# Kernel tuning notes

Hardware: AMD Instinct MI355X
Metric: run time of the kernel (lower is better)

## Reference

```python
import jax, jax.numpy as jnp
import numpy as np

B = 256          # graphs per batch
N = 128          # nodes per graph (equal-size graphs; batch is block-contiguous)
P = N * (N - 1) // 2  # pairs per graph = 8128
E = B * 1024     # total edges
D = 128          # node feature dim
L = 32           # latent dim

# precomputed local upper-triangular pair indices (constants)
_PI, _PJ = np.triu_indices(N, k=1)
_PI = jnp.asarray(_PI); _PJ = jnp.asarray(_PJ)


def setup_inputs() -> dict:
    key = jax.random.key(0)
    ks = jax.random.split(key, 8)
    x = jax.random.normal(ks[0], (B * N, D), dtype=jnp.float32)
    # within-graph edges with local i < j
    li = jax.random.randint(ks[1], (E,), 0, N - 1)
    r = jax.random.randint(ks[2], (E,), 0, 1 << 30)
    lj = li + 1 + r % (N - 1 - li)
    g = jax.random.randint(ks[3], (E,), 0, B)
    off = g * N
    edge_index = jnp.stack([off + li, off + lj]).astype(jnp.int64)
    batch = jnp.repeat(jnp.arange(B), N).astype(jnp.int64)
    eps = jax.random.normal(ks[4], (B * N, L), dtype=jnp.float32)
    W1 = jax.random.normal(ks[5], (D, D), dtype=jnp.float32) * 0.05
    b1 = jnp.zeros((D,), dtype=jnp.float32)
    Wmu = jax.random.normal(ks[6], (D, L), dtype=jnp.float32) * 0.05
    bmu = jnp.zeros((L,), dtype=jnp.float32)
    Wls = jax.random.normal(ks[7], (D, L), dtype=jnp.float32) * 0.05
    bls = jnp.zeros((L,), dtype=jnp.float32)
    return {"x": x, "edge_index": edge_index, "batch": batch, "eps": eps,
            "W1": W1, "b1": b1, "Wmu": Wmu, "bmu": bmu, "Wls": Wls, "bls": bls}


def reference(x, edge_index, batch, eps, W1, b1, Wmu, bmu, Wls, bls):
    src, dst = edge_index[0], edge_index[1]
    # --- encoder: one symmetric message-passing layer -> Gaussian q per node ---
    agg = jnp.zeros_like(x).at[dst].add(x[src]).at[src].add(x[dst])
    h = jax.nn.relu((x + agg) @ W1 + b1)
    mu = h @ Wmu + bmu                       # [BN, L]
    log_std = h @ Wls + bls
    std = jnp.exp(log_std)
    z = mu + std * eps                       # rsample
    # --- KL(q || N(0,I)) per node, summed per graph (kls[b]) ---
    kl_node = 0.5 * jnp.sum(std * std + mu * mu - 1.0 - 2.0 * log_std, axis=-1)
    kls = jax.ops.segment_sum(kl_node, batch, num_segments=B)  # [B]
    # --- link targets: scatter edges into triangular pair slots ---
    li, lj, be = src % N, dst % N, src // N
    pidx = li * (2 * N - li - 1) // 2 + (lj - li - 1)
    targets = jnp.zeros((B, P), dtype=z.dtype).at[be, pidx].set(1.0)
    # --- inner-product Bernoulli decoder over all pairs of every graph ---
    zb = z.reshape(B, N, L)
    logits = jnp.einsum('bpl,bpl->bp', zb[:, _PI], zb[:, _PJ])   # [B, P]
    log_probs = jnp.sum(targets * logits - jax.nn.softplus(logits), axis=-1)  # [B]
    elbo = jnp.mean(log_probs - kls)
    return -elbo
```

## Files before the change

kernel.cpp:

```cpp
#include <hip/hip_runtime.h>
#include <math.h>

#define B_ 256
#define N_ 128
#define D_ 128
#define L_ 32
#define E_ 262144
#define PW_ 254
#define DCAP 96

#define NDEG_OFF 0
#define BM_OFF   32768
#define KLS_OFF  97792
#define LP_OFF   98048
#define ADJ_OFF  98304
#define Z_OFF    884736
#define ZERO_WORDS 98304

__global__ __launch_bounds__(256) void k_build(
    const int* __restrict__ ei, unsigned* __restrict__ ndeg,
    unsigned char* __restrict__ adj, unsigned* __restrict__ bm)
{
    int e = blockIdx.x * 256 + threadIdx.x;
    int src = ei[e], dst = ei[E_ + e];
    unsigned s1 = atomicAdd(&ndeg[src], 1u);
    if (s1 < DCAP) adj[(size_t)src * DCAP + s1] = (unsigned char)(dst & 127);
    unsigned s2 = atomicAdd(&ndeg[dst], 1u);
    if (s2 < DCAP) adj[(size_t)dst * DCAP + s2] = (unsigned char)(src & 127);
    int li = src & 127, lj = dst & 127, g = src >> 7;
    int p = li * (255 - li) / 2 + (lj - li - 1);
    atomicOr(&bm[g * PW_ + (p >> 5)], 1u << (p & 31));
}

__global__ __launch_bounds__(256, 4) void k_encoder(
    const float* __restrict__ x, const unsigned* __restrict__ ndeg,
    const unsigned char* __restrict__ adj,
    const float* __restrict__ W1, const float* __restrict__ b1,
    const float* __restrict__ Wmu, const float* __restrict__ bmu,
    const float* __restrict__ Wls, const float* __restrict__ bls,
    const float* __restrict__ eps,
    float* __restrict__ z, float* __restrict__ kls)
{
    __shared__ float XAs[32 * 132];
    __shared__ float Ws[4096];
    int t = threadIdx.x;
    int g = blockIdx.x & 255;
    int quar = blockIdx.x >> 8;
    int row0 = g * 128 + quar * 32;
    int rg = t >> 5;
    int cg = t & 31;
    int lane = t & 63;

    {
        int nidx = t >> 4;
        int fo = (t & 15) * 8;
        for (int p = 0; p < 2; ++p) {
            int lrow = p * 16 + nidx;
            int gnode = row0 + lrow;
            const float* xr = x + (size_t)gnode * 128 + fo;
            float4 a0 = *(const float4*)xr;
            float4 a1 = *(const float4*)(xr + 4);
            int deg = (int)ndeg[gnode];
            if (deg > DCAP) deg = DCAP;
            const unsigned char* al = adj + (size_t)gnode * DCAP;
            const float* gx = x + (size_t)(gnode & ~127) * 128 + fo;
            int e = 0;
            for (; e + 4 <= deg; e += 4) {
                unsigned pk = *(const unsigned*)(al + e);
                const float* r0 = gx + (pk & 255u) * 128;
                const float* r1 = gx + ((pk >> 8) & 255u) * 128;
                const float* r2 = gx + ((pk >> 16) & 255u) * 128;
                const float* r3 = gx + (pk >> 24) * 128;
                float4 v00 = *(const float4*)r0, v01 = *(const float4*)(r0 + 4);
                float4 v10 = *(const float4*)r1, v11 = *(const float4*)(r1 + 4);
                float4 v20 = *(const float4*)r2, v21 = *(const float4*)(r2 + 4);
                float4 v30 = *(const float4*)r3, v31 = *(const float4*)(r3 + 4);
                a0.x += v00.x + v10.x + v20.x + v30.x;
                a0.y += v00.y + v10.y + v20.y + v30.y;
                a0.z += v00.z + v10.z + v20.z + v30.z;
                a0.w += v00.w + v10.w + v20.w + v30.w;
                a1.x += v01.x + v11.x + v21.x + v31.x;
                a1.y += v01.y + v11.y + v21.y + v31.y;
                a1.z += v01.z + v11.z + v21.z + v31.z;
                a1.w += v01.w + v11.w + v21.w + v31.w;
            }
            for (; e < deg; ++e) {
                const float* r = gx + (unsigned)al[e] * 128;
                float4 v0 = *(const float4*)r, v1 = *(const float4*)(r + 4);
                a0.x += v0.x; a0.y += v0.y; a0.z += v0.z; a0.w += v0.w;
                a1.x += v1.x; a1.y += v1.y; a1.z += v1.z; a1.w += v1.w;
            }
            *(float4*)(XAs + lrow * 132 + fo) = a0;
            *(float4*)(XAs + lrow * 132 + fo + 4) = a1;
        }
    }
    __syncthreads();

    float acc[4][4];
    #pragma unroll
    for (int i = 0; i < 4; ++i)
        #pragma unroll
        for (int j = 0; j < 4; ++j) acc[i][j] = 0.f;

    for (int kq = 0; kq < 4; ++kq) {
        if (kq) __syncthreads();
        #pragma unroll
        for (int i = 0; i < 4; ++i) {
            int c = t + i * 256;
            ((float4*)Ws)[c] = ((const float4*)(W1 + kq * 4096))[c];
        }
        __syncthreads();
        #pragma unroll 2
        for (int k = 0; k < 32; k += 4) {
            float4 av[4], wv[4];
            #pragma unroll
            for (int i = 0; i < 4; ++i)
                av[i] = *(const float4*)(XAs + (4 * rg + i) * 132 + kq * 32 + k);
            #pragma unroll
            for (int dk = 0; dk < 4; ++dk)
                wv[dk] = *(const float4*)(Ws + (k + dk) * 128 + 4 * cg);
            #pragma unroll
            for (int i = 0; i < 4; ++i) {
                acc[i][0] += av[i].x * wv[0].x + av[i].y * wv[1].x + av[i].z * wv[2].x + av[i].w * wv[3].x;
                acc[i][1] += av[i].x * wv[0].y + av[i].y * wv[1].y + av[i].z * wv[2].y + av[i].w * wv[3].y;
                acc[i][2] += av[i].x * wv[0].z + av[i].y * wv[1].z + av[i].z * wv[2].z + av[i].w * wv[3].z;
                acc[i][3] += av[i].x * wv[0].w + av[i].y * wv[1].w + av[i].z * wv[2].w + av[i].w * wv[3].w;
            }
        }
    }
    __syncthreads();

    {
        float4 bb = *(const float4*)(b1 + 4 * cg);
        #pragma unroll
        for (int i = 0; i < 4; ++i) {
            float4 h;
            h.x = fmaxf(acc[i][0] + bb.x, 0.f);
            h.y = fmaxf(acc[i][1] + bb.y, 0.f);
            h.z = fmaxf(acc[i][2] + bb.z, 0.f);
            h.w = fmaxf(acc[i][3] + bb.w, 0.f);
            *(float4*)(XAs + (4 * rg + i) * 132 + 4 * cg) = h;
        }
    }

    float a3[4][2];
    #pragma unroll
    for (int i = 0; i < 4; ++i) { a3[i][0] = 0.f; a3[i][1] = 0.f; }

    for (int kh = 0; kh < 2; ++kh) {
        __syncthreads();
        #pragma unroll
        for (int i = 0; i < 4; ++i) {
            int c = t + i * 256;
            int row = c >> 4, col4 = (c & 15) << 2;
            int rowg = kh * 64 + row;
            float4 v = (col4 < 32) ? *(const float4*)(Wmu + rowg * 32 + col4)
                                   : *(const float4*)(Wls + rowg * 32 + col4 - 32);
            *(float4*)(Ws + row * 64 + col4) = v;
        }
        __syncthreads();
        #pragma unroll 2
        for (int k = 0; k < 64; k += 4) {
            float4 av[4];
            float2 wv[4];
            #pragma unroll
            for (int i = 0; i < 4; ++i)
                av[i] = *(const float4*)(XAs + (4 * rg + i) * 132 + kh * 64 + k);
            #pragma unroll
            for (int dk = 0; dk < 4; ++dk)
                wv[dk] = *(const float2*)(Ws + (k + dk) * 64 + 2 * cg);
            #pragma unroll
            for (int i = 0; i < 4; ++i) {
                a3[i][0] += av[i].x * wv[0].x + av[i].y * wv[1].x + av[i].z * wv[2].x + av[i].w * wv[3].x;
                a3[i][1] += av[i].x * wv[0].y + av[i].y * wv[1].y + av[i].z * wv[2].y + av[i].w * wv[3].y;
            }
        }
    }
    {
        float2 bv = (cg < 16) ? *(const float2*)(bmu + 2 * cg)
                              : *(const float2*)(bls + 2 * cg - 32);
        #pragma unroll
        for (int i = 0; i < 4; ++i) { a3[i][0] += bv.x; a3[i][1] += bv.y; }
    }

    float o3[4][2];
    #pragma unroll
    for (int i = 0; i < 4; ++i) {
        o3[i][0] = __shfl_xor(a3[i][0], 16);
        o3[i][1] = __shfl_xor(a3[i][1], 16);
    }

    float klsum = 0.f;
    if (cg < 16) {
        int lo = cg;
        #pragma unroll
        for (int i = 0; i < 4; ++i) {
            int rowg = row0 + 4 * rg + i;
            float mu0 = a3[i][0], mu1 = a3[i][1];
            float ls0 = o3[i][0], ls1 = o3[i][1];
            float2 ev = *(const float2*)(eps + (size_t)rowg * 32 + 2 * lo);
            float s0 = __expf(ls0), s1 = __expf(ls1);
            float2 zv = make_float2(mu0 + s0 * ev.x, mu1 + s1 * ev.y);
            *(float2*)(z + (size_t)rowg * 32 + 2 * lo) = zv;
            klsum += s0 * s0 + mu0 * mu0 - 1.f - 2.f * ls0
                   + s1 * s1 + mu1 * mu1 - 1.f - 2.f * ls1;
        }
    }
    #pragma unroll
    for (int off = 32; off > 0; off >>= 1) klsum += __shfl_xor(klsum, off);
    if (lane == 0) atomicAdd(&kls[g], 0.5f * klsum);
}

__global__ __launch_bounds__(256) void k_decoder(
    const float* __restrict__ z, const unsigned* __restrict__ bitmap,
    float* __restrict__ logp)
{
    __shared__ float zT[32 * 132];
    __shared__ unsigned bm[PW_];
    int b = blockIdx.x & 255, quar = blockIdx.x >> 8, t = threadIdx.x;

    #pragma unroll
    for (int i = 0; i < 16; ++i) {
        int c = t + i * 256;
        int n = c >> 5, l = c & 31;
        zT[l * 132 + n] = z[((size_t)b * N_ + n) * L_ + l];
    }
    if (t < PW_) bm[t] = bitmap[b * PW_ + t];
    __syncthreads();

    int i0 = quar * 32 + ((t >> 5) << 2);
    int j0 = (t & 31) << 2;
    float g[4][4];
    #pragma unroll
    for (int a = 0; a < 4; ++a)
        #pragma unroll
        for (int c = 0; c < 4; ++c) g[a][c] = 0.f;

    #pragma unroll 4
    for (int l = 0; l < 32; ++l) {
        float4 a0 = *(const float4*)(zT + l * 132 + i0);
        float4 b0 = *(const float4*)(zT + l * 132 + j0);
        float za[4] = {a0.x, a0.y, a0.z, a0.w};
        float zb[4] = {b0.x, b0.y, b0.z, b0.w};
        #pragma unroll
        for (int a = 0; a < 4; ++a)
            #pragma unroll
            for (int c = 0; c < 4; ++c) g[a][c] += za[a] * zb[c];
    }

    float sum = 0.f;
    #pragma unroll
    for (int a = 0; a < 4; ++a) {
        int i = i0 + a;
        #pragma unroll
        for (int c = 0; c < 4; ++c) {
            int j = j0 + c;
            if (j > i) {
                float lg = g[a][c];
                int p = i * (255 - i) / 2 + (j - i - 1);
                unsigned bit = (bm[p >> 5] >> (p & 31)) & 1u;
                float sp = __logf(1.f + __expf(-fabsf(lg))) + fmaxf(lg, 0.f);
                sum += bit ? (lg - sp) : (-sp);
            }
        }
    }
    #pragma unroll
    for (int off = 32; off > 0; off >>= 1) sum += __shfl_xor(sum, off);
    if ((t & 63) == 0) atomicAdd(&logp[b], sum);
}

__global__ __launch_bounds__(256) void k_finalize(
    const float* __restrict__ kls, const float* __restrict__ logp,
    float* __restrict__ out)
{
    __shared__ float RED[256];
    int t = threadIdx.x;
    RED[t] = logp[t] - kls[t];
    __syncthreads();
    for (int s = 128; s > 0; s >>= 1) {
        if (t < s) RED[t] += RED[t + s];
        __syncthreads();
    }
    if (t == 0) out[0] = -RED[0] * (1.0f / 256.0f);
}

extern "C" void kernel_launch(void* const* d_in, const int* in_sizes, int n_in,
                              void* d_out, int out_size, void* d_ws, size_t ws_size,
                              hipStream_t stream) {
    const float* x   = (const float*)d_in[0];
    const int*   ei  = (const int*)d_in[1];
    const float* eps = (const float*)d_in[3];
    const float* W1  = (const float*)d_in[4];
    const float* b1  = (const float*)d_in[5];
    const float* Wmu = (const float*)d_in[6];
    const float* bmu = (const float*)d_in[7];
    const float* Wls = (const float*)d_in[8];
    const float* bls = (const float*)d_in[9];

    unsigned* wsw = (unsigned*)d_ws;
    unsigned*      ndeg = wsw + NDEG_OFF;
    unsigned*      bm   = wsw + BM_OFF;
    float*         kls  = (float*)(wsw + KLS_OFF);
    float*         logp = (float*)(wsw + LP_OFF);
    unsigned char* adj  = (unsigned char*)(wsw + ADJ_OFF);
    float*         z    = (float*)(wsw + Z_OFF);

    hipMemsetAsync(d_ws, 0, ZERO_WORDS * sizeof(unsigned), stream);

    k_build   <<<E_ / 256, 256, 0, stream>>>(ei, ndeg, adj, bm);
    k_encoder <<<1024, 256, 0, stream>>>(x, ndeg, adj, W1, b1, Wmu, bmu,
                                         Wls, bls, eps, z, kls);
    k_decoder <<<4 * B_, 256, 0, stream>>>(z, bm, logp);
    k_finalize<<<1, 256, 0, stream>>>(kls, logp, (float*)d_out);
}
```

Before: 175.2 us.

## Read encoder weights from global directly, fuse finalize into decoder via last-block counter

The encoder no longer stages W1 and Wmu/Wls through shared memory. Each thread reads weight vectors straight from global/L2, which removes several barriers and the 16KB shared buffer, and the occupancy hint rises to 6 blocks per SM. The decoder loads z with float4 reads, and the separate finalize kernel is replaced by a done counter: the last decoder block to finish performs the final reduction. This saves a kernel launch and shared-memory traffic, at the cost of redundant global weight loads per block and a relaxed-ordering last-block pattern.

```diff
diff --git a/kernel.cpp b/kernel.cpp
--- a/kernel.cpp
+++ b/kernel.cpp
@@ -13,9 +13,10 @@
 #define BM_OFF   32768
 #define KLS_OFF  97792
 #define LP_OFF   98048
-#define ADJ_OFF  98304
-#define Z_OFF    884736
-#define ZERO_WORDS 98304
+#define DONE_OFF 98304
+#define ADJ_OFF  98320
+#define Z_OFF    884752
+#define ZERO_WORDS 98320
 
 __global__ __launch_bounds__(256) void k_build(
     const int* __restrict__ ei, unsigned* __restrict__ ndeg,
@@ -32,7 +33,7 @@
     atomicOr(&bm[g * PW_ + (p >> 5)], 1u << (p & 31));
 }
 
-__global__ __launch_bounds__(256, 4) void k_encoder(
+__global__ __launch_bounds__(256, 6) void k_encoder(
     const float* __restrict__ x, const unsigned* __restrict__ ndeg,
     const unsigned char* __restrict__ adj,
     const float* __restrict__ W1, const float* __restrict__ b1,
@@ -42,7 +43,6 @@
     float* __restrict__ z, float* __restrict__ kls)
 {
     __shared__ float XAs[32 * 132];
-    __shared__ float Ws[4096];
     int t = threadIdx.x;
     int g = blockIdx.x & 255;
     int quar = blockIdx.x >> 8;
@@ -102,23 +102,17 @@
         #pragma unroll
         for (int j = 0; j < 4; ++j) acc[i][j] = 0.f;
 
-    for (int kq = 0; kq < 4; ++kq) {
-        if (kq) __syncthreads();
-        #pragma unroll
-        for (int i = 0; i < 4; ++i) {
-            int c = t + i * 256;
-            ((float4*)Ws)[c] = ((const float4*)(W1 + kq * 4096))[c];
-        }
-        __syncthreads();
+    {
+        const float* Wp = W1 + 4 * cg;
         #pragma unroll 2
-        for (int k = 0; k < 32; k += 4) {
+        for (int k = 0; k < 128; k += 4) {
             float4 av[4], wv[4];
             #pragma unroll
             for (int i = 0; i < 4; ++i)
-                av[i] = *(const float4*)(XAs + (4 * rg + i) * 132 + kq * 32 + k);
+                av[i] = *(const float4*)(XAs + (4 * rg + i) * 132 + k);
             #pragma unroll
             for (int dk = 0; dk < 4; ++dk)
-                wv[dk] = *(const float4*)(Ws + (k + dk) * 128 + 4 * cg);
+                wv[dk] = *(const float4*)(Wp + (k + dk) * 128);
             #pragma unroll
             for (int i = 0; i < 4; ++i) {
                 acc[i][0] += av[i].x * wv[0].x + av[i].y * wv[1].x + av[i].z * wv[2].x + av[i].w * wv[3].x;
@@ -128,7 +122,6 @@
             }
         }
     }
-    __syncthreads();
 
     {
         float4 bb = *(const float4*)(b1 + 4 * cg);
@@ -142,33 +135,24 @@
             *(float4*)(XAs + (4 * rg + i) * 132 + 4 * cg) = h;
         }
     }
+    __syncthreads();
 
     float a3[4][2];
     #pragma unroll
     for (int i = 0; i < 4; ++i) { a3[i][0] = 0.f; a3[i][1] = 0.f; }
 
-    for (int kh = 0; kh < 2; ++kh) {
-        __syncthreads();
-        #pragma unroll
-        for (int i = 0; i < 4; ++i) {
-            int c = t + i * 256;
-            int row = c >> 4, col4 = (c & 15) << 2;
-            int rowg = kh * 64 + row;
-            float4 v = (col4 < 32) ? *(const float4*)(Wmu + rowg * 32 + col4)
-                                   : *(const float4*)(Wls + rowg * 32 + col4 - 32);
-            *(float4*)(Ws + row * 64 + col4) = v;
-        }
-        __syncthreads();
+    {
+        const float* W2p = (cg < 16) ? (Wmu + 2 * cg) : (Wls + 2 * (cg - 16));
         #pragma unroll 2
-        for (int k = 0; k < 64; k += 4) {
+        for (int k = 0; k < 128; k += 4) {
             float4 av[4];
             float2 wv[4];
             #pragma unroll
             for (int i = 0; i < 4; ++i)
-                av[i] = *(const float4*)(XAs + (4 * rg + i) * 132 + kh * 64 + k);
+                av[i] = *(const float4*)(XAs + (4 * rg + i) * 132 + k);
             #pragma unroll
             for (int dk = 0; dk < 4; ++dk)
-                wv[dk] = *(const float2*)(Ws + (k + dk) * 64 + 2 * cg);
+                wv[dk] = *(const float2*)(W2p + (k + dk) * 32);
             #pragma unroll
             for (int i = 0; i < 4; ++i) {
                 a3[i][0] += av[i].x * wv[0].x + av[i].y * wv[1].x + av[i].z * wv[2].x + av[i].w * wv[3].x;
@@ -213,28 +197,34 @@
 
 __global__ __launch_bounds__(256) void k_decoder(
     const float* __restrict__ z, const unsigned* __restrict__ bitmap,
-    float* __restrict__ logp)
+    float* __restrict__ logp, const float* __restrict__ kls,
+    unsigned* __restrict__ done, float* __restrict__ out)
 {
     __shared__ float zT[32 * 132];
     __shared__ unsigned bm[PW_];
+    __shared__ unsigned lastflag;
     int b = blockIdx.x & 255, quar = blockIdx.x >> 8, t = threadIdx.x;
 
     #pragma unroll
-    for (int i = 0; i < 16; ++i) {
+    for (int i = 0; i < 4; ++i) {
         int c = t + i * 256;
-        int n = c >> 5, l = c & 31;
-        zT[l * 132 + n] = z[((size_t)b * N_ + n) * L_ + l];
+        int n = c >> 3, l = (c & 7) << 2;
+        float4 v = *(const float4*)(z + ((size_t)b * N_ + n) * L_ + l);
+        zT[(l + 0) * 132 + n] = v.x;
+        zT[(l + 1) * 132 + n] = v.y;
+        zT[(l + 2) * 132 + n] = v.z;
+        zT[(l + 3) * 132 + n] = v.w;
     }
     if (t < PW_) bm[t] = bitmap[b * PW_ + t];
     __syncthreads();
 
     int i0 = quar * 32 + ((t >> 5) << 2);
     int j0 = (t & 31) << 2;
-    float g[4][4];
+    float gacc[4][4];
     #pragma unroll
     for (int a = 0; a < 4; ++a)
         #pragma unroll
-        for (int c = 0; c < 4; ++c) g[a][c] = 0.f;
+        for (int c = 0; c < 4; ++c) gacc[a][c] = 0.f;
 
     #pragma unroll 4
     for (int l = 0; l < 32; ++l) {
@@ -245,7 +235,7 @@
         #pragma unroll
         for (int a = 0; a < 4; ++a)
             #pragma unroll
-            for (int c = 0; c < 4; ++c) g[a][c] += za[a] * zb[c];
+            for (int c = 0; c < 4; ++c) gacc[a][c] += za[a] * zb[c];
     }
 
     float sum = 0.f;
@@ -256,7 +246,7 @@
         for (int c = 0; c < 4; ++c) {
             int j = j0 + c;
             if (j > i) {
-                float lg = g[a][c];
+                float lg = gacc[a][c];
                 int p = i * (255 - i) / 2 + (j - i - 1);
                 unsigned bit = (bm[p >> 5] >> (p & 31)) & 1u;
                 float sp = __logf(1.f + __expf(-fabsf(lg))) + fmaxf(lg, 0.f);
@@ -267,21 +257,24 @@
     #pragma unroll
     for (int off = 32; off > 0; off >>= 1) sum += __shfl_xor(sum, off);
     if ((t & 63) == 0) atomicAdd(&logp[b], sum);
-}
-
-__global__ __launch_bounds__(256) void k_finalize(
-    const float* __restrict__ kls, const float* __restrict__ logp,
-    float* __restrict__ out)
-{
-    __shared__ float RED[256];
-    int t = threadIdx.x;
-    RED[t] = logp[t] - kls[t];
-    __syncthreads();
-    for (int s = 128; s > 0; s >>= 1) {
-        if (t < s) RED[t] += RED[t + s];
+
+    __syncthreads();
+    if (t == 0) {
+        unsigned prev = atomicAdd(done, 1u);
+        lastflag = (prev == 4u * B_ - 1u) ? 1u : 0u;
+    }
+    __syncthreads();
+    if (lastflag) {
+        float v = __hip_atomic_load(&logp[t], __ATOMIC_RELAXED, __HIP_MEMORY_SCOPE_AGENT)
+                - __hip_atomic_load(&kls[t],  __ATOMIC_RELAXED, __HIP_MEMORY_SCOPE_AGENT);
+        zT[t] = v;
         __syncthreads();
-    }
-    if (t == 0) out[0] = -RED[0] * (1.0f / 256.0f);
+        for (int s = 128; s > 0; s >>= 1) {
+            if (t < s) zT[t] += zT[t + s];
+            __syncthreads();
+        }
+        if (t == 0) out[0] = -zT[0] * (1.0f / 256.0f);
+    }
 }
 
 extern "C" void kernel_launch(void* const* d_in, const int* in_sizes, int n_in,
@@ -302,6 +295,7 @@
     unsigned*      bm   = wsw + BM_OFF;
     float*         kls  = (float*)(wsw + KLS_OFF);
     float*         logp = (float*)(wsw + LP_OFF);
+    unsigned*      done = wsw + DONE_OFF;
     unsigned char* adj  = (unsigned char*)(wsw + ADJ_OFF);
     float*         z    = (float*)(wsw + Z_OFF);
 
@@ -310,6 +304,5 @@
     k_build   <<<E_ / 256, 256, 0, stream>>>(ei, ndeg, adj, bm);
     k_encoder <<<1024, 256, 0, stream>>>(x, ndeg, adj, W1, b1, Wmu, bmu,
                                          Wls, bls, eps, z, kls);
-    k_decoder <<<4 * B_, 256, 0, stream>>>(z, bm, logp);
-    k_finalize<<<1, 256, 0, stream>>>(kls, logp, (float*)d_out);
+    k_decoder <<<4 * B_, 256, 0, stream>>>(z, bm, logp, kls, done, (float*)d_out);
 }
```

Result: slower. 194.3 us (+10.9%).

## Fuse build, encoder, decoder and finalize into one persistent kernel with grid barriers

Applied to the files above, without the earlier changes.

Merges the four separate kernel launches into a single kernel of 1024 blocks. Phases are separated by software grid-wide barriers built on an atomic counter in workspace with acquire/release semantics. The aim is to remove the launch overhead and inter-kernel gaps between the four dependent stages. The barriers assume all 1024 blocks are co-resident (256 CUs times 4 blocks); if they are not, the kernel deadlocks. The spin waits also add latency.

```diff
diff --git a/kernel.cpp b/kernel.cpp
--- a/kernel.cpp
+++ b/kernel.cpp
@@ -8,280 +8,306 @@
 #define E_ 262144
 #define PW_ 254
 #define DCAP 96
+#define GRID_ 1024
 
 #define NDEG_OFF 0
 #define BM_OFF   32768
 #define KLS_OFF  97792
 #define LP_OFF   98048
-#define ADJ_OFF  98304
-#define Z_OFF    884736
-#define ZERO_WORDS 98304
-
-__global__ __launch_bounds__(256) void k_build(
-    const int* __restrict__ ei, unsigned* __restrict__ ndeg,
-    unsigned char* __restrict__ adj, unsigned* __restrict__ bm)
-{
-    int e = blockIdx.x * 256 + threadIdx.x;
-    int src = ei[e], dst = ei[E_ + e];
-    unsigned s1 = atomicAdd(&ndeg[src], 1u);
-    if (s1 < DCAP) adj[(size_t)src * DCAP + s1] = (unsigned char)(dst & 127);
-    unsigned s2 = atomicAdd(&ndeg[dst], 1u);
-    if (s2 < DCAP) adj[(size_t)dst * DCAP + s2] = (unsigned char)(src & 127);
-    int li = src & 127, lj = dst & 127, g = src >> 7;
-    int p = li * (255 - li) / 2 + (lj - li - 1);
-    atomicOr(&bm[g * PW_ + (p >> 5)], 1u << (p & 31));
-}
-
-__global__ __launch_bounds__(256, 4) void k_encoder(
-    const float* __restrict__ x, const unsigned* __restrict__ ndeg,
-    const unsigned char* __restrict__ adj,
+#define BAR_OFF  98304
+#define ADJ_OFF  98320
+#define Z_OFF    884752
+#define ZERO_WORDS 98320
+
+__global__ __launch_bounds__(256, 4) void k_fused(
+    const float* __restrict__ x, const int* __restrict__ ei,
+    const float* __restrict__ eps,
     const float* __restrict__ W1, const float* __restrict__ b1,
     const float* __restrict__ Wmu, const float* __restrict__ bmu,
     const float* __restrict__ Wls, const float* __restrict__ bls,
-    const float* __restrict__ eps,
-    float* __restrict__ z, float* __restrict__ kls)
+    unsigned* ndeg, unsigned* bmg,
+    float* kls, float* logp, unsigned* bar,
+    unsigned char* adj, float* z, float* out)
 {
-    __shared__ float XAs[32 * 132];
-    __shared__ float Ws[4096];
+    __shared__ float SM[8320];
     int t = threadIdx.x;
-    int g = blockIdx.x & 255;
-    int quar = blockIdx.x >> 8;
-    int row0 = g * 128 + quar * 32;
-    int rg = t >> 5;
-    int cg = t & 31;
-    int lane = t & 63;
+    int blk = blockIdx.x;
 
     {
-        int nidx = t >> 4;
-        int fo = (t & 15) * 8;
-        for (int p = 0; p < 2; ++p) {
-            int lrow = p * 16 + nidx;
-            int gnode = row0 + lrow;
-            const float* xr = x + (size_t)gnode * 128 + fo;
-            float4 a0 = *(const float4*)xr;
-            float4 a1 = *(const float4*)(xr + 4);
-            int deg = (int)ndeg[gnode];
-            if (deg > DCAP) deg = DCAP;
-            const unsigned char* al = adj + (size_t)gnode * DCAP;
-            const float* gx = x + (size_t)(gnode & ~127) * 128 + fo;
-            int e = 0;
-            for (; e + 4 <= deg; e += 4) {
-                unsigned pk = *(const unsigned*)(al + e);
-                const float* r0 = gx + (pk & 255u) * 128;
-                const float* r1 = gx + ((pk >> 8) & 255u) * 128;
-                const float* r2 = gx + ((pk >> 16) & 255u) * 128;
-                const float* r3 = gx + (pk >> 24) * 128;
-                float4 v00 = *(const float4*)r0, v01 = *(const float4*)(r0 + 4);
-                float4 v10 = *(const float4*)r1, v11 = *(const float4*)(r1 + 4);
-                float4 v20 = *(const float4*)r2, v21 = *(const float4*)(r2 + 4);
-                float4 v30 = *(const float4*)r3, v31 = *(const float4*)(r3 + 4);
-                a0.x += v00.x + v10.x + v20.x + v30.x;
-                a0.y += v00.y + v10.y + v20.y + v30.y;
-                a0.z += v00.z + v10.z + v20.z + v30.z;
-                a0.w += v00.w + v10.w + v20.w + v30.w;
-                a1.x += v01.x + v11.x + v21.x + v31.x;
-                a1.y += v01.y + v11.y + v21.y + v31.y;
-                a1.z += v01.z + v11.z + v21.z + v31.z;
-                a1.w += v01.w + v11.w + v21.w + v31.w;
-            }
-            for (; e < deg; ++e) {
-                const float* r = gx + (unsigned)al[e] * 128;
-                float4 v0 = *(const float4*)r, v1 = *(const float4*)(r + 4);
-                a0.x += v0.x; a0.y += v0.y; a0.z += v0.z; a0.w += v0.w;
-                a1.x += v1.x; a1.y += v1.y; a1.z += v1.z; a1.w += v1.w;
-            }
-            *(float4*)(XAs + lrow * 132 + fo) = a0;
-            *(float4*)(XAs + lrow * 132 + fo + 4) = a1;
-        }
-    }
-    __syncthreads();
-
-    float acc[4][4];
-    #pragma unroll
-    for (int i = 0; i < 4; ++i)
-        #pragma unroll
-        for (int j = 0; j < 4; ++j) acc[i][j] = 0.f;
-
-    for (int kq = 0; kq < 4; ++kq) {
-        if (kq) __syncthreads();
+        int e = blk * 256 + t;
+        int src = ei[e], dst = ei[E_ + e];
+        unsigned s1 = atomicAdd(&ndeg[src], 1u);
+        if (s1 < DCAP) adj[(size_t)src * DCAP + s1] = (unsigned char)(dst & 127);
+        unsigned s2 = atomicAdd(&ndeg[dst], 1u);
+        if (s2 < DCAP) adj[(size_t)dst * DCAP + s2] = (unsigned char)(src & 127);
+        int li = src & 127, lj = dst & 127, gg = src >> 7;
+        int p = li * (255 - li) / 2 + (lj - li - 1);
+        atomicOr(&bmg[gg * PW_ + (p >> 5)], 1u << (p & 31));
+    }
+
+    __syncthreads();
+    if (t == 0) {
+        __hip_atomic_fetch_add(bar, 1u, __ATOMIC_ACQ_REL, __HIP_MEMORY_SCOPE_AGENT);
+        while (__hip_atomic_load(bar, __ATOMIC_RELAXED, __HIP_MEMORY_SCOPE_AGENT) < 1u * GRID_)
+            __builtin_amdgcn_s_sleep(4);
+        (void)__hip_atomic_load(bar, __ATOMIC_ACQUIRE, __HIP_MEMORY_SCOPE_AGENT);
+    }
+    __syncthreads();
+
+    {
+        float* XAs = SM;
+        float* Ws  = SM + 4224;
+        int g = blk & 255;
+        int quar = blk >> 8;
+        int row0 = g * 128 + quar * 32;
+        int rg = t >> 5;
+        int cg_ = t & 31;
+        int lane = t & 63;
+
+        {
+            int nidx = t >> 4;
+            int fo = (t & 15) * 8;
+            for (int p = 0; p < 2; ++p) {
+                int lrow = p * 16 + nidx;
+                int gnode = row0 + lrow;
+                const float* xr = x + (size_t)gnode * 128 + fo;
+                float4 a0 = *(const float4*)xr;
+                float4 a1 = *(const float4*)(xr + 4);
+                int deg = (int)ndeg[gnode];
+                if (deg > DCAP) deg = DCAP;
+                const unsigned char* al = adj + (size_t)gnode * DCAP;
+                const float* gx = x + (size_t)(gnode & ~127) * 128 + fo;
+                int e = 0;
+                for (; e + 4 <= deg; e += 4) {
+                    unsigned pk = *(const unsigned*)(al + e);
+                    const float* r0 = gx + (pk & 255u) * 128;
+                    const float* r1 = gx + ((pk >> 8) & 255u) * 128;
+                    const float* r2 = gx + ((pk >> 16) & 255u) * 128;
+                    const float* r3 = gx + (pk >> 24) * 128;
+                    float4 v00 = *(const float4*)r0, v01 = *(const float4*)(r0 + 4);
+                    float4 v10 = *(const float4*)r1, v11 = *(const float4*)(r1 + 4);
+                    float4 v20 = *(const float4*)r2, v21 = *(const float4*)(r2 + 4);
+                    float4 v30 = *(const float4*)r3, v31 = *(const float4*)(r3 + 4);
+                    a0.x += v00.x + v10.x + v20.x + v30.x;
+                    a0.y += v00.y + v10.y + v20.y + v30.y;
+                    a0.z += v00.z + v10.z + v20.z + v30.z;
+                    a0.w += v00.w + v10.w + v20.w + v30.w;
+                    a1.x += v01.x + v11.x + v21.x + v31.x;
+                    a1.y += v01.y + v11.y + v21.y + v31.y;
+                    a1.z += v01.z + v11.z + v21.z + v31.z;
+                    a1.w += v01.w + v11.w + v21.w + v31.w;
+                }
+                for (; e < deg; ++e) {
+                    const float* r = gx + (unsigned)al[e] * 128;
+                    float4 v0 = *(const float4*)r, v1 = *(const float4*)(r + 4);
+                    a0.x += v0.x; a0.y += v0.y; a0.z += v0.z; a0.w += v0.w;
+                    a1.x += v1.x; a1.y += v1.y; a1.z += v1.z; a1.w += v1.w;
+                }
+                *(float4*)(XAs + lrow * 132 + fo) = a0;
+                *(float4*)(XAs + lrow * 132 + fo + 4) = a1;
+            }
+        }
+        __syncthreads();
+
+        float acc[4][4];
+        #pragma unroll
+        for (int i = 0; i < 4; ++i)
+            #pragma unroll
+            for (int j = 0; j < 4; ++j) acc[i][j] = 0.f;
+
+        for (int kq = 0; kq < 4; ++kq) {
+            if (kq) __syncthreads();
+            #pragma unroll
+            for (int i = 0; i < 4; ++i) {
+                int c = t + i * 256;
+                ((float4*)Ws)[c] = ((const float4*)(W1 + kq * 4096))[c];
+            }
+            __syncthreads();
+            #pragma unroll 2
+            for (int k = 0; k < 32; k += 4) {
+                float4 av[4], wv[4];
+                #pragma unroll
+                for (int i = 0; i < 4; ++i)
+                    av[i] = *(const float4*)(XAs + (4 * rg + i) * 132 + kq * 32 + k);
+                #pragma unroll
+                for (int dk = 0; dk < 4; ++dk)
+                    wv[dk] = *(const float4*)(Ws + (k + dk) * 128 + 4 * cg_);
+                #pragma unroll
+                for (int i = 0; i < 4; ++i) {
+                    acc[i][0] += av[i].x * wv[0].x + av[i].y * wv[1].x + av[i].z * wv[2].x + av[i].w * wv[3].x;
+                    acc[i][1] += av[i].x * wv[0].y + av[i].y * wv[1].y + av[i].z * wv[2].y + av[i].w * wv[3].y;
+                    acc[i][2] += av[i].x * wv[0].z + av[i].y * wv[1].z + av[i].z * wv[2].z + av[i].w * wv[3].z;
+                    acc[i][3] += av[i].x * wv[0].w + av[i].y * wv[1].w + av[i].z * wv[2].w + av[i].w * wv[3].w;
+                }
+            }
+        }
+        __syncthreads();
+
+        {
+            float4 bb = *(const float4*)(b1 + 4 * cg_);
+            #pragma unroll
+            for (int i = 0; i < 4; ++i) {
+                float4 h;
+                h.x = fmaxf(acc[i][0] + bb.x, 0.f);
+                h.y = fmaxf(acc[i][1] + bb.y, 0.f);
+                h.z = fmaxf(acc[i][2] + bb.z, 0.f);
+                h.w = fmaxf(acc[i][3] + bb.w, 0.f);
+                *(float4*)(XAs + (4 * rg + i) * 132 + 4 * cg_) = h;
+            }
+        }
+
+        float a3[4][2];
+        #pragma unroll
+        for (int i = 0; i < 4; ++i) { a3[i][0] = 0.f; a3[i][1] = 0.f; }
+
+        for (int kh = 0; kh < 2; ++kh) {
+            __syncthreads();
+            #pragma unroll
+            for (int i = 0; i < 4; ++i) {
+                int c = t + i * 256;
+                int row = c >> 4, col4 = (c & 15) << 2;
+                int rowg = kh * 64 + row;
+                float4 v = (col4 < 32) ? *(const float4*)(Wmu + rowg * 32 + col4)
+                                       : *(const float4*)(Wls + rowg * 32 + col4 - 32);
+                *(float4*)(Ws + row * 64 + col4) = v;
+            }
+            __syncthreads();
+            #pragma unroll 2
+            for (int k = 0; k < 64; k += 4) {
+                float4 av[4];
+                float2 wv[4];
+                #pragma unroll
+                for (int i = 0; i < 4; ++i)
+                    av[i] = *(const float4*)(XAs + (4 * rg + i) * 132 + kh * 64 + k);
+                #pragma unroll
+                for (int dk = 0; dk < 4; ++dk)
+                    wv[dk] = *(const float2*)(Ws + (k + dk) * 64 + 2 * cg_);
+                #pragma unroll
+                for (int i = 0; i < 4; ++i) {
+                    a3[i][0] += av[i].x * wv[0].x + av[i].y * wv[1].x + av[i].z * wv[2].x + av[i].w * wv[3].x;
+                    a3[i][1] += av[i].x * wv[0].y + av[i].y * wv[1].y + av[i].z * wv[2].y + av[i].w * wv[3].y;
+                }
+            }
+        }
+        {
+            float2 bv = (cg_ < 16) ? *(const float2*)(bmu + 2 * cg_)
+                                   : *(const float2*)(bls + 2 * cg_ - 32);
+            #pragma unroll
+            for (int i = 0; i < 4; ++i) { a3[i][0] += bv.x; a3[i][1] += bv.y; }
+        }
+
+        float o3[4][2];
         #pragma unroll
         for (int i = 0; i < 4; ++i) {
+            o3[i][0] = __shfl_xor(a3[i][0], 16);
+            o3[i][1] = __shfl_xor(a3[i][1], 16);
+        }
+
+        float klsum = 0.f;
+        if (cg_ < 16) {
+            int lo = cg_;
+            #pragma unroll
+            for (int i = 0; i < 4; ++i) {
+                int rowg = row0 + 4 * rg + i;
+                float mu0 = a3[i][0], mu1 = a3[i][1];
+                float ls0 = o3[i][0], ls1 = o3[i][1];
+                float2 ev = *(const float2*)(eps + (size_t)rowg * 32 + 2 * lo);
+                float s0 = __expf(ls0), s1 = __expf(ls1);
+                float2 zv = make_float2(mu0 + s0 * ev.x, mu1 + s1 * ev.y);
+                *(float2*)(z + (size_t)rowg * 32 + 2 * lo) = zv;
+                klsum += s0 * s0 + mu0 * mu0 - 1.f - 2.f * ls0
+                       + s1 * s1 + mu1 * mu1 - 1.f - 2.f * ls1;
+            }
+        }
+        #pragma unroll
+        for (int off = 32; off > 0; off >>= 1) klsum += __shfl_xor(klsum, off);
+        if (lane == 0) atomicAdd(&kls[g], 0.5f * klsum);
+    }
+
+    __syncthreads();
+    if (t == 0) {
+        __hip_atomic_fetch_add(bar, 1u, __ATOMIC_ACQ_REL, __HIP_MEMORY_SCOPE_AGENT);
+        while (__hip_atomic_load(bar, __ATOMIC_RELAXED, __HIP_MEMORY_SCOPE_AGENT) < 2u * GRID_)
+            __builtin_amdgcn_s_sleep(4);
+        (void)__hip_atomic_load(bar, __ATOMIC_ACQUIRE, __HIP_MEMORY_SCOPE_AGENT);
+    }
+    __syncthreads();
+
+    {
+        float* zT = SM;
+        unsigned* bmS = (unsigned*)(SM + 4224);
+        int b = blk & 255, quar = blk >> 8;
+
+        #pragma unroll
+        for (int i = 0; i < 16; ++i) {
             int c = t + i * 256;
-            ((float4*)Ws)[c] = ((const float4*)(W1 + kq * 4096))[c];
-        }
+            int n = c >> 5, l = c & 31;
+            zT[l * 132 + n] = z[((size_t)b * N_ + n) * L_ + l];
+        }
+        if (t < PW_) bmS[t] = bmg[b * PW_ + t];
         __syncthreads();
-        #pragma unroll 2
-        for (int k = 0; k < 32; k += 4) {
-            float4 av[4], wv[4];
-            #pragma unroll
-            for (int i = 0; i < 4; ++i)
-                av[i] = *(const float4*)(XAs + (4 * rg + i) * 132 + kq * 32 + k);
-            #pragma unroll
-            for (int dk = 0; dk < 4; ++dk)
-                wv[dk] = *(const float4*)(Ws + (k + dk) * 128 + 4 * cg);
-            #pragma unroll
-            for (int i = 0; i < 4; ++i) {
-                acc[i][0] += av[i].x * wv[0].x + av[i].y * wv[1].x + av[i].z * wv[2].x + av[i].w * wv[3].x;
-                acc[i][1] += av[i].x * wv[0].y + av[i].y * wv[1].y + av[i].z * wv[2].y + av[i].w * wv[3].y;
-                acc[i][2] += av[i].x * wv[0].z + av[i].y * wv[1].z + av[i].z * wv[2].z + av[i].w * wv[3].z;
-                acc[i][3] += av[i].x * wv[0].w + av[i].y * wv[1].w + av[i].z * wv[2].w + av[i].w * wv[3].w;
-            }
-        }
-    }
-    __syncthreads();
-
+
+        int i0 = quar * 32 + ((t >> 5) << 2);
+        int j0 = (t & 31) << 2;
+        float gacc[4][4];
+        #pragma unroll
+        for (int a = 0; a < 4; ++a)
+            #pragma unroll
+            for (int c = 0; c < 4; ++c) gacc[a][c] = 0.f;
+
+        #pragma unroll 4
+        for (int l = 0; l < 32; ++l) {
+            float4 a0 = *(const float4*)(zT + l * 132 + i0);
+            float4 b0 = *(const float4*)(zT + l * 132 + j0);
+            float za[4] = {a0.x, a0.y, a0.z, a0.w};
+            float zb[4] = {b0.x, b0.y, b0.z, b0.w};
+            #pragma unroll
+            for (int a = 0; a < 4; ++a)
+                #pragma unroll
+                for (int c = 0; c < 4; ++c) gacc[a][c] += za[a] * zb[c];
+        }
+
+        float sum = 0.f;
+        #pragma unroll
+        for (int a = 0; a < 4; ++a) {
+            int i = i0 + a;
+            #pragma unroll
+            for (int c = 0; c < 4; ++c) {
+                int j = j0 + c;
+                if (j > i) {
+                    float lg = gacc[a][c];
+                    int p = i * (255 - i) / 2 + (j - i - 1);
+                    unsigned bit = (bmS[p >> 5] >> (p & 31)) & 1u;
+                    float sp = __logf(1.f + __expf(-fabsf(lg))) + fmaxf(lg, 0.f);
+                    sum += bit ? (lg - sp) : (-sp);
+                }
+            }
+        }
+        #pragma unroll
+        for (int off = 32; off > 0; off >>= 1) sum += __shfl_xor(sum, off);
+        if ((t & 63) == 0) atomicAdd(&logp[b], sum);
+    }
+
+    __syncthreads();
+    if (t == 0)
+        __hip_atomic_fetch_add(bar, 1u, __ATOMIC_ACQ_REL, __HIP_MEMORY_SCOPE_AGENT);
+    if (blk != 0) return;
+    if (t == 0) {
+        while (__hip_atomic_load(bar, __ATOMIC_RELAXED, __HIP_MEMORY_SCOPE_AGENT) < 3u * GRID_)
+            __builtin_amdgcn_s_sleep(4);
+        (void)__hip_atomic_load(bar, __ATOMIC_ACQUIRE, __HIP_MEMORY_SCOPE_AGENT);
+    }
+    __syncthreads();
     {
-        float4 bb = *(const float4*)(b1 + 4 * cg);
-        #pragma unroll
-        for (int i = 0; i < 4; ++i) {
-            float4 h;
-            h.x = fmaxf(acc[i][0] + bb.x, 0.f);
-            h.y = fmaxf(acc[i][1] + bb.y, 0.f);
-            h.z = fmaxf(acc[i][2] + bb.z, 0.f);
-            h.w = fmaxf(acc[i][3] + bb.w, 0.f);
-            *(float4*)(XAs + (4 * rg + i) * 132 + 4 * cg) = h;
-        }
-    }
-
-    float a3[4][2];
-    #pragma unroll
-    for (int i = 0; i < 4; ++i) { a3[i][0] = 0.f; a3[i][1] = 0.f; }
-
-    for (int kh = 0; kh < 2; ++kh) {
+        float* RED = SM;
+        RED[t] = logp[t] - kls[t];
         __syncthreads();
-        #pragma unroll
-        for (int i = 0; i < 4; ++i) {
-            int c = t + i * 256;
-            int row = c >> 4, col4 = (c & 15) << 2;
-            int rowg = kh * 64 + row;
-            float4 v = (col4 < 32) ? *(const float4*)(Wmu + rowg * 32 + col4)
-                                   : *(const float4*)(Wls + rowg * 32 + col4 - 32);
-            *(float4*)(Ws + row * 64 + col4) = v;
-        }
-        __syncthreads();
-        #pragma unroll 2
-        for (int k = 0; k < 64; k += 4) {
-            float4 av[4];
-            float2 wv[4];
-            #pragma unroll
-            for (int i = 0; i < 4; ++i)
-                av[i] = *(const float4*)(XAs + (4 * rg + i) * 132 + kh * 64 + k);
-            #pragma unroll
-            for (int dk = 0; dk < 4; ++dk)
-                wv[dk] = *(const float2*)(Ws + (k + dk) * 64 + 2 * cg);
-            #pragma unroll
-            for (int i = 0; i < 4; ++i) {
-                a3[i][0] += av[i].x * wv[0].x + av[i].y * wv[1].x + av[i].z * wv[2].x + av[i].w * wv[3].x;
-                a3[i][1] += av[i].x * wv[0].y + av[i].y * wv[1].y + av[i].z * wv[2].y + av[i].w * wv[3].y;
-            }
-        }
-    }
-    {
-        float2 bv = (cg < 16) ? *(const float2*)(bmu + 2 * cg)
-                              : *(const float2*)(bls + 2 * cg - 32);
-        #pragma unroll
-        for (int i = 0; i < 4; ++i) { a3[i][0] += bv.x; a3[i][1] += bv.y; }
-    }
-
-    float o3[4][2];
-    #pragma unroll
-    for (int i = 0; i < 4; ++i) {
-        o3[i][0] = __shfl_xor(a3[i][0], 16);
-        o3[i][1] = __shfl_xor(a3[i][1], 16);
-    }
-
-    float klsum = 0.f;
-    if (cg < 16) {
-        int lo = cg;
-        #pragma unroll
-        for (int i = 0; i < 4; ++i) {
-            int rowg = row0 + 4 * rg + i;
-            float mu0 = a3[i][0], mu1 = a3[i][1];
-            float ls0 = o3[i][0], ls1 = o3[i][1];
-            float2 ev = *(const float2*)(eps + (size_t)rowg * 32 + 2 * lo);
-            float s0 = __expf(ls0), s1 = __expf(ls1);
-            float2 zv = make_float2(mu0 + s0 * ev.x, mu1 + s1 * ev.y);
-            *(float2*)(z + (size_t)rowg * 32 + 2 * lo) = zv;
-            klsum += s0 * s0 + mu0 * mu0 - 1.f - 2.f * ls0
-                   + s1 * s1 + mu1 * mu1 - 1.f - 2.f * ls1;
-        }
-    }
-    #pragma unroll
-    for (int off = 32; off > 0; off >>= 1) klsum += __shfl_xor(klsum, off);
-    if (lane == 0) atomicAdd(&kls[g], 0.5f * klsum);
-}
-
-__global__ __launch_bounds__(256) void k_decoder(
-    const float* __restrict__ z, const unsigned* __restrict__ bitmap,
-    float* __restrict__ logp)
-{
-    __shared__ float zT[32 * 132];
-    __shared__ unsigned bm[PW_];
-    int b = blockIdx.x & 255, quar = blockIdx.x >> 8, t = threadIdx.x;
-
-    #pragma unroll
-    for (int i = 0; i < 16; ++i) {
-        int c = t + i * 256;
-        int n = c >> 5, l = c & 31;
-        zT[l * 132 + n] = z[((size_t)b * N_ + n) * L_ + l];
-    }
-    if (t < PW_) bm[t] = bitmap[b * PW_ + t];
-    __syncthreads();
-
-    int i0 = quar * 32 + ((t >> 5) << 2);
-    int j0 = (t & 31) << 2;
-    float g[4][4];
-    #pragma unroll
-    for (int a = 0; a < 4; ++a)
-        #pragma unroll
-        for (int c = 0; c < 4; ++c) g[a][c] = 0.f;
-
-    #pragma unroll 4
-    for (int l = 0; l < 32; ++l) {
-        float4 a0 = *(const float4*)(zT + l * 132 + i0);
-        float4 b0 = *(const float4*)(zT + l * 132 + j0);
-        float za[4] = {a0.x, a0.y, a0.z, a0.w};
-        float zb[4] = {b0.x, b0.y, b0.z, b0.w};
-        #pragma unroll
-        for (int a = 0; a < 4; ++a)
-            #pragma unroll
-            for (int c = 0; c < 4; ++c) g[a][c] += za[a] * zb[c];
-    }
-
-    float sum = 0.f;
-    #pragma unroll
-    for (int a = 0; a < 4; ++a) {
-        int i = i0 + a;
-        #pragma unroll
-        for (int c = 0; c < 4; ++c) {
-            int j = j0 + c;
-            if (j > i) {
-                float lg = g[a][c];
-                int p = i * (255 - i) / 2 + (j - i - 1);
-                unsigned bit = (bm[p >> 5] >> (p & 31)) & 1u;
-                float sp = __logf(1.f + __expf(-fabsf(lg))) + fmaxf(lg, 0.f);
-                sum += bit ? (lg - sp) : (-sp);
-            }
-        }
-    }
-    #pragma unroll
-    for (int off = 32; off > 0; off >>= 1) sum += __shfl_xor(sum, off);
-    if ((t & 63) == 0) atomicAdd(&logp[b], sum);
-}
-
-__global__ __launch_bounds__(256) void k_finalize(
-    const float* __restrict__ kls, const float* __restrict__ logp,
-    float* __restrict__ out)
-{
-    __shared__ float RED[256];
-    int t = threadIdx.x;
-    RED[t] = logp[t] - kls[t];
-    __syncthreads();
-    for (int s = 128; s > 0; s >>= 1) {
-        if (t < s) RED[t] += RED[t + s];
-        __syncthreads();
-    }
-    if (t == 0) out[0] = -RED[0] * (1.0f / 256.0f);
+        for (int s = 128; s > 0; s >>= 1) {
+            if (t < s) RED[t] += RED[t + s];
+            __syncthreads();
+        }
+        if (t == 0) out[0] = -RED[0] * (1.0f / 256.0f);
+    }
 }
 
 extern "C" void kernel_launch(void* const* d_in, const int* in_sizes, int n_in,
@@ -302,14 +328,13 @@
     unsigned*      bm   = wsw + BM_OFF;
     float*         kls  = (float*)(wsw + KLS_OFF);
     float*         logp = (float*)(wsw + LP_OFF);
+    unsigned*      bar  = wsw + BAR_OFF;
     unsigned char* adj  = (unsigned char*)(wsw + ADJ_OFF);
     float*         z    = (float*)(wsw + Z_OFF);
 
     hipMemsetAsync(d_ws, 0, ZERO_WORDS * sizeof(unsigned), stream);
 
-    k_build   <<<E_ / 256, 256, 0, stream>>>(ei, ndeg, adj, bm);
-    k_encoder <<<1024, 256, 0, stream>>>(x, ndeg, adj, W1, b1, Wmu, bmu,
-                                         Wls, bls, eps, z, kls);
-    k_decoder <<<4 * B_, 256, 0, stream>>>(z, bm, logp);
-    k_finalize<<<1, 256, 0, stream>>>(kls, logp, (float*)d_out);
+    k_fused<<<GRID_, 256, 0, stream>>>(x, ei, eps, W1, b1, Wmu, bmu, Wls, bls,
+                                       ndeg, bm, kls, logp, bar, adj, z,
+                                       (float*)d_out);
 }
```

Result: slower. 379.1 us (+116.4%).
